# Kernel tuning notes

Measured on AMD Instinct MI355X. Metric: run time of the kernel, lower is better.

## Reference

```python
import jax, jax.numpy as jnp
import numpy as np

B, S, HID, NH = 2, 2048, 1024, 16
HD = HID // NH  # 64


def setup_inputs() -> dict:
    key = jax.random.key(0)
    ks = jax.random.split(key, 10)
    sc = 0.02
    return {
        "hidden_states": jax.random.normal(ks[0], (B, S, HID), jnp.float32),
        "attention_mask": jnp.zeros((B, 1, 1, S), jnp.float32),
        "struct_attn_mask": jax.random.normal(ks[1], (B, S, S), jnp.float32),
        "Wq": jax.random.normal(ks[2], (HID, HID), jnp.float32) * sc,
        "bq": jnp.zeros((HID,), jnp.float32),
        "Wk": jax.random.normal(ks[3], (HID, HID), jnp.float32) * sc,
        "bk": jnp.zeros((HID,), jnp.float32),
        "Wv": jax.random.normal(ks[4], (HID, HID), jnp.float32) * sc,
        "bv": jnp.zeros((HID,), jnp.float32),
        "struct_gate": jnp.full((NH,), 0.1, jnp.float32),
    }


def _heads(x):
    # [B,S,HID] -> [B,NH,S,HD]
    return x.reshape(B, S, NH, HD).transpose(0, 2, 1, 3)


def reference(hidden_states, attention_mask, struct_attn_mask, Wq, bq, Wk, bk, Wv, bv, struct_gate):
    q = _heads(hidden_states @ Wq.T + bq)
    k = _heads(hidden_states @ Wk.T + bk)
    v = _heads(hidden_states @ Wv.T + bv)
    scores = jnp.einsum("bhqd,bhkd->bhqk", q, k) / np.sqrt(HD).astype(np.float32)
    scores = scores + attention_mask
    scores = scores + struct_attn_mask[:, None, :, :] * struct_gate[None, :, None, None]
    probs = jax.nn.softmax(scores, axis=-1)  # dropout p=0 (eval) -> no-op
    ctx = jnp.einsum("bhqk,bhkd->bhqd", probs, v)
    ctx = ctx.transpose(0, 2, 1, 3).reshape(B, S, HID)
    return (ctx,)
```

## Files before the change

### kernel.cpp

```cpp
#include <hip/hip_runtime.h>
#include <hip/hip_bf16.h>
#include <cmath>

#define S_LEN 2048
#define HIDN  1024
#define NHEAD 16
#define HDIM  64
#define NBAT  2

static constexpr long NA = (long)NBAT * S_LEN * HIDN;
static constexpr long NW = (long)HIDN * HIDN;
static constexpr long NM = (long)NBAT * S_LEN * S_LEN;
static constexpr long NAM = (long)NBAT * S_LEN;

typedef __attribute__((ext_vector_type(8))) __bf16 bf16x8;
typedef __attribute__((ext_vector_type(4))) float f32x4;
typedef __attribute__((ext_vector_type(16))) float f32x16;
typedef __attribute__((ext_vector_type(4))) unsigned short u16x4;

#define LOG2E 1.44269504088896340736f

__device__ __forceinline__ unsigned short f2bf(float f) {
  __hip_bfloat16 h = __float2bfloat16(f);
  unsigned short u;
  __builtin_memcpy(&u, &h, 2);
  return u;
}

__device__ __forceinline__ float bfu2f(unsigned short u) {
  unsigned v = (unsigned)u << 16;
  float f;
  __builtin_memcpy(&f, &v, 4);
  return f;
}

__device__ __forceinline__ unsigned cvtpk(float a, float b) {
  unsigned r;
  asm volatile("v_cvt_pk_bf16_f32 %0, %1, %2" : "=v"(r) : "v"(a), "v"(b));
  return r;
}

__device__ __forceinline__ void gload_lds16(const void* g, void* l) {
  __builtin_amdgcn_global_load_lds(
      (const __attribute__((address_space(1))) void*)g,
      (__attribute__((address_space(3))) void*)l, 16, 0, 0);
}

__global__ __launch_bounds__(256) void convert_kernel(
    const float* __restrict__ hs, const float* __restrict__ wq,
    const float* __restrict__ wk, const float* __restrict__ wv,
    const float* __restrict__ mask, const float* __restrict__ amask,
    __hip_bfloat16* __restrict__ Abf, __hip_bfloat16* __restrict__ Wcat,
    __hip_bfloat16* __restrict__ Mbf, float* __restrict__ amg) {
  const long tot4 = (NA + 3 * NW + NM + NAM) >> 2;
  for (long i4 = (long)blockIdx.x * blockDim.x + threadIdx.x; i4 < tot4;
       i4 += (long)gridDim.x * blockDim.x) {
    long i = i4 << 2;
    if (i < NA + 3 * NW + NM) {
      const float* s;
      __hip_bfloat16* dq;
      if (i < NA)               { s = hs + i;                   dq = Abf + i; }
      else if (i < NA + NW)     { s = wq + (i - NA);            dq = Wcat + (i - NA); }
      else if (i < NA + 2 * NW) { s = wk + (i - NA - NW);       dq = Wcat + (i - NA); }
      else if (i < NA + 3 * NW) { s = wv + (i - NA - 2 * NW);   dq = Wcat + (i - NA); }
      else                      { s = mask + (i - NA - 3 * NW); dq = Mbf + (i - NA - 3 * NW); }
      float4 v = *(const float4*)s;
      union { unsigned short u[4]; uint2 p; } o;
      o.u[0] = f2bf(v.x); o.u[1] = f2bf(v.y); o.u[2] = f2bf(v.z); o.u[3] = f2bf(v.w);
      *(uint2*)dq = o.p;
    } else {
      long j = i - (NA + 3 * NW + NM);
      float4 v = *(const float4*)(amask + j);
      v.x *= LOG2E; v.y *= LOG2E; v.z *= LOG2E; v.w *= LOG2E;
      *(float4*)(amg + j) = v;
    }
  }
}

__global__ __launch_bounds__(256) void qkv_gemm(
    const __hip_bfloat16* __restrict__ A, const __hip_bfloat16* __restrict__ Bw,
    const float* __restrict__ bq, const float* __restrict__ bk,
    const float* __restrict__ bv, __hip_bfloat16* __restrict__ qb,
    __hip_bfloat16* __restrict__ kb, __hip_bfloat16* __restrict__ vb) {
  __shared__ __hip_bfloat16 sA[128 * 32];
  __shared__ __hip_bfloat16 sB[128 * 32];

  int bid = blockIdx.x;
  int cpx = gridDim.x >> 3;
  int wg = (bid & 7) * cpx + (bid >> 3);
  int bm = wg / 24, bn = wg % 24;
  int tid = threadIdx.x, lane = tid & 63, wid = tid >> 6;
  int wr = wid >> 1, wc = wid & 1;
  int lr = lane & 15, hi = lane >> 4;
  int srow = lane >> 2, scol = (lane & 3) * 8;

  f32x4 acc[4][4] = {};

  for (int kt = 0; kt < 32; ++kt) {
    int k0 = kt * 32;
#pragma unroll
    for (int cc = 0; cc < 2; ++cc) {
      int c = wid * 2 + cc;
      const __hip_bfloat16* ga =
          A + ((size_t)(bm * 128 + c * 16 + srow) * 1024 + k0 + scol);
      gload_lds16(ga, (char*)sA + c * 1024);
      const __hip_bfloat16* gb =
          Bw + ((size_t)(bn * 128 + c * 16 + srow) * 1024 + k0 + scol);
      gload_lds16(gb, (char*)sB + c * 1024);
    }
    __syncthreads();
    bf16x8 af[4], bf[4];
#pragma unroll
    for (int mt = 0; mt < 4; ++mt)
      af[mt] = *(const bf16x8*)((const char*)sA +
                                ((wr * 64 + mt * 16 + lr) * 32 + hi * 8) * 2);
#pragma unroll
    for (int nt = 0; nt < 4; ++nt)
      bf[nt] = *(const bf16x8*)((const char*)sB +
                                ((wc * 64 + nt * 16 + lr) * 32 + hi * 8) * 2);
#pragma unroll
    for (int mt = 0; mt < 4; ++mt)
#pragma unroll
      for (int nt = 0; nt < 4; ++nt)
        acc[mt][nt] =
            __builtin_amdgcn_mfma_f32_16x16x32_bf16(af[mt], bf[nt], acc[mt][nt], 0, 0, 0);
    __syncthreads();
  }

  const float c2 = LOG2E / 8.0f;
#pragma unroll
  for (int nt = 0; nt < 4; ++nt) {
    int nb = bn * 128 + wc * 64 + nt * 16;
    int t = nb >> 10;
    int rem = nb & 1023;
    const float* bp = (t == 0) ? bq : (t == 1) ? bk : bv;
    __hip_bfloat16* ob = (t == 0) ? qb : (t == 1) ? kb : vb;
    float scl = (t == 0) ? c2 : 1.0f;
    int h = rem >> 6, d0 = rem & 63;
    float bias = bp[rem + lr];
    int d = d0 + lr;
#pragma unroll
    for (int mt = 0; mt < 4; ++mt) {
#pragma unroll
      for (int r = 0; r < 4; ++r) {
        int m = bm * 128 + wr * 64 + mt * 16 + hi * 4 + r;
        int b = m >> 11, s = m & 2047;
        size_t off = (((size_t)(b * NHEAD + h)) * S_LEN + s) * HDIM + d;
        ob[off] = __float2bfloat16((acc[mt][nt][r] + bias) * scl);
      }
    }
  }
}

__global__ __launch_bounds__(256) void vtrans_kernel(
    const __hip_bfloat16* __restrict__ vb, __hip_bfloat16* __restrict__ vt) {
  __shared__ __hip_bfloat16 tile[64][72];
  int bh = blockIdx.x >> 5;
  int st = blockIdx.x & 31;
  int t = threadIdx.x;
  int r8 = t >> 3, c8 = (t & 7) * 8;
#pragma unroll
  for (int p = 0; p < 2; ++p) {
    int row = p * 32 + r8;
    bf16x8 v = *(const bf16x8*)(vb + ((size_t)bh * S_LEN + st * 64 + row) * HDIM + c8);
    *(bf16x8*)&tile[row][c8] = v;
  }
  __syncthreads();
#pragma unroll
  for (int p = 0; p < 2; ++p) {
    int d = p * 32 + r8;
    union { unsigned short u[8]; bf16x8 v; } o;
#pragma unroll
    for (int j = 0; j < 8; ++j) {
      __hip_bfloat16 e = tile[c8 + j][d];
      __builtin_memcpy(&o.u[j], &e, 2);
    }
    *(bf16x8*)(vt + ((size_t)bh * HDIM + d) * S_LEN + st * 64 + c8) = o.v;
  }
}

__global__ __launch_bounds__(512, 4) void attn_kernel(
    const __hip_bfloat16* __restrict__ qb, const __hip_bfloat16* __restrict__ kbuf,
    const __hip_bfloat16* __restrict__ vt, const __hip_bfloat16* __restrict__ Mbf,
    const float* __restrict__ amg, const float* __restrict__ gate,
    float* __restrict__ out) {
  __shared__ alignas(16) char smem[65536];
  __shared__ float mlb[4][2][32];

  int bid = blockIdx.x;
  int wg = (bid & 7) * 64 + (bid >> 3);
  int bi = wg >> 8;
  int h = (wg >> 4) & 15;
  int qt = wg & 15;
  int bh = bi * NHEAD + h;

  int tid = threadIdx.x;
  int lane = tid & 63, wid = tid >> 6;
  int grp = wid >> 2, w4 = wid & 3;
  int l31 = lane & 31, hi2 = lane >> 5;
  int qbase = qt * 128 + w4 * 32;
  int qrow = qbase + l31;
  int kbase = grp << 10;
  float g2 = gate[h] * LOG2E;

  const char* Kb = (const char*)kbuf + (size_t)bh * S_LEN * 128;
  const char* Vb = (const char*)vt + (size_t)bh * HDIM * S_LEN * 2;
  const char* Mq = (const char*)Mbf + ((size_t)bi * S_LEN + qbase) * S_LEN * 2;
  const float* abase = amg + (size_t)bi * S_LEN + hi2 * 4;

  bf16x8 qf[4];
  {
    const __hip_bfloat16* qp = qb + ((size_t)bh * S_LEN + qrow) * HDIM + hi2 * 8;
#pragma unroll
    for (int dc = 0; dc < 4; ++dc) qf[dc] = *(const bf16x8*)(qp + dc * 16);
  }

  int r8 = lane >> 3;
  int swzK = ((lane & 7) ^ r8) << 4;
  int r4 = lane >> 2;
  int swz64 = ((lane & 3) ^ (r4 & 3)) << 4;

  auto stage = [&](int buf, int t) {
    int k0 = kbase + t * 32;
    char* base = smem + buf * 8192 + grp * 4096 + w4 * 1024;
    gload_lds16(Kb + (size_t)(k0 + w4 * 8 + r8) * 128 + swzK, base);
    gload_lds16(Vb + (size_t)(w4 * 16 + r4) * 4096 + (size_t)k0 * 2 + swz64,
                base + 16384);
    char* mdst = smem + 32768 + buf * 16384 + wid * 2048;
#pragma unroll
    for (int c = 0; c < 2; ++c) {
      int mrow = c * 16 + r4;
      gload_lds16(Mq + (size_t)mrow * 4096 + (size_t)k0 * 2 + swz64,
                  mdst + c * 1024);
    }
  };

  f32x16 O = {};
  f32x16 O2 = {};
  float m = -INFINITY, l = 0.f;
  int rswzK = (l31 & 7) << 4;
  int rswz64 = (l31 & 3) << 4;

  stage(0, 0);
  __syncthreads();

  for (int kt = 0; kt < 32; ++kt) {
    int cur = kt & 1;
    if (kt < 31) stage(cur ^ 1, kt + 1);
    int k0 = kbase + kt * 32;

    const char* sKc = smem + cur * 8192 + grp * 4096;
    const char* sVc = sKc + 16384;
    const char* sMc = smem + 32768 + cur * 16384 + wid * 2048;

    f32x16 st = {};
#pragma unroll
    for (int dc = 0; dc < 4; ++dc) {
      bf16x8 kf = *(const bf16x8*)(sKc + l31 * 128 + ((dc * 32 + hi2 * 16) ^ rswzK));
      st = __builtin_amdgcn_mfma_f32_32x32x16_bf16(kf, qf[dc], st, 0, 0, 0);
    }

    float pmax = -3.4e38f;
#pragma unroll
    for (int rp = 0; rp < 4; ++rp) {
      float4 am = *(const float4*)(abase + k0 + rp * 8);
      union { u16x4 v; unsigned short e[4]; } mv;
      mv.v = *(const u16x4*)(sMc + l31 * 64 + ((rp * 16) ^ rswz64) + hi2 * 8);
      float s0 = fmaf(bfu2f(mv.e[0]), g2, st[rp * 4 + 0] + am.x);
      float s1 = fmaf(bfu2f(mv.e[1]), g2, st[rp * 4 + 1] + am.y);
      float s2 = fmaf(bfu2f(mv.e[2]), g2, st[rp * 4 + 2] + am.z);
      float s3 = fmaf(bfu2f(mv.e[3]), g2, st[rp * 4 + 3] + am.w);
      st[rp * 4 + 0] = s0; st[rp * 4 + 1] = s1;
      st[rp * 4 + 2] = s2; st[rp * 4 + 3] = s3;
      pmax = fmaxf(pmax, fmaxf(fmaxf(s0, s1), fmaxf(s2, s3)));
    }
    pmax = fmaxf(pmax, __shfl_xor(pmax, 32));

    if (__any(pmax > m + 8.f)) {
      float mnew = fmaxf(m, pmax);
      float alpha = exp2f(m - mnew);
      m = mnew;
      l *= alpha;
      O *= alpha;
      O2 *= alpha;
    }

    float rs0 = 0.f, rs1 = 0.f, rs2 = 0.f, rs3 = 0.f;
#pragma unroll
    for (int rp = 0; rp < 4; ++rp) {
      float p0 = exp2f(st[rp * 4 + 0] - m);
      float p1 = exp2f(st[rp * 4 + 1] - m);
      float p2 = exp2f(st[rp * 4 + 2] - m);
      float p3 = exp2f(st[rp * 4 + 3] - m);
      st[rp * 4 + 0] = p0; st[rp * 4 + 1] = p1;
      st[rp * 4 + 2] = p2; st[rp * 4 + 3] = p3;
      rs0 += p0; rs1 += p1; rs2 += p2; rs3 += p3;
    }
    float rs = (rs0 + rs1) + (rs2 + rs3);
    rs += __shfl_xor(rs, 32);
    l += rs;

#pragma unroll
    for (int ks = 0; ks < 2; ++ks) {
      int rp = ks * 2;
      unsigned A0 = cvtpk(st[rp * 4 + 0], st[rp * 4 + 1]);
      unsigned A1 = cvtpk(st[rp * 4 + 2], st[rp * 4 + 3]);
      unsigned B0 = cvtpk(st[rp * 4 + 4], st[rp * 4 + 5]);
      unsigned B1 = cvtpk(st[rp * 4 + 6], st[rp * 4 + 7]);
      asm volatile("v_permlane32_swap_b32 %0, %1" : "+v"(A0), "+v"(B0));
      asm volatile("v_permlane32_swap_b32 %0, %1" : "+v"(A1), "+v"(B1));
      union { unsigned w[4]; bf16x8 v; } Bf;
      Bf.w[0] = A0; Bf.w[1] = A1; Bf.w[2] = B0; Bf.w[3] = B1;
      bf16x8 v0 = *(const bf16x8*)(sVc + l31 * 64 + (((ks * 2 + hi2) << 4) ^ rswz64));
      bf16x8 v1 = *(const bf16x8*)(sVc + (32 + l31) * 64 + (((ks * 2 + hi2) << 4) ^ rswz64));
      O = __builtin_amdgcn_mfma_f32_32x32x16_bf16(v0, Bf.v, O, 0, 0, 0);
      O2 = __builtin_amdgcn_mfma_f32_32x32x16_bf16(v1, Bf.v, O2, 0, 0, 0);
    }
    __syncthreads();
  }

  float* mbuf = (float*)smem + w4 * (32 * 68);
  if (grp == 1) {
    if (hi2 == 0) { mlb[w4][0][l31] = m; mlb[w4][1][l31] = l; }
#pragma unroll
    for (int dt = 0; dt < 2; ++dt)
#pragma unroll
      for (int rq = 0; rq < 4; ++rq) {
        int d0 = dt * 32 + 8 * rq + 4 * hi2;
        const f32x16& Ox = dt ? O2 : O;
        f32x4 v = {Ox[rq * 4 + 0], Ox[rq * 4 + 1], Ox[rq * 4 + 2], Ox[rq * 4 + 3]};
        *(f32x4*)(mbuf + l31 * 68 + d0) = v;
      }
  }
  __syncthreads();
  if (grp == 0) {
    float m1 = mlb[w4][0][l31], l1 = mlb[w4][1][l31];
    float mx = fmaxf(m, m1);
    float a0 = exp2f(m - mx), a1 = exp2f(m1 - mx);
    float linv = 1.0f / (a0 * l + a1 * l1);
    a0 *= linv; a1 *= linv;
    float* orow = out + ((size_t)bi * S_LEN + qrow) * HIDN + h * HDIM;
#pragma unroll
    for (int dt = 0; dt < 2; ++dt)
#pragma unroll
      for (int rq = 0; rq < 4; ++rq) {
        int d0 = dt * 32 + 8 * rq + 4 * hi2;
        const f32x16& Ox = dt ? O2 : O;
        f32x4 v1 = *(const f32x4*)(mbuf + l31 * 68 + d0);
        float4 o;
        o.x = Ox[rq * 4 + 0] * a0 + v1[0] * a1;
        o.y = Ox[rq * 4 + 1] * a0 + v1[1] * a1;
        o.z = Ox[rq * 4 + 2] * a0 + v1[2] * a1;
        o.w = Ox[rq * 4 + 3] * a0 + v1[3] * a1;
        *(float4*)(orow + d0) = o;
      }
  }
}

extern "C" void kernel_launch(void* const* d_in, const int* in_sizes, int n_in,
                              void* d_out, int out_size, void* d_ws, size_t ws_size,
                              hipStream_t stream) {
  const float* hs    = (const float*)d_in[0];
  const float* amask = (const float*)d_in[1];
  const float* smask = (const float*)d_in[2];
  const float* Wq    = (const float*)d_in[3];
  const float* bq    = (const float*)d_in[4];
  const float* Wk    = (const float*)d_in[5];
  const float* bk    = (const float*)d_in[6];
  const float* Wv    = (const float*)d_in[7];
  const float* bv    = (const float*)d_in[8];
  const float* gate  = (const float*)d_in[9];

  char* ws = (char*)d_ws;
  __hip_bfloat16* Abf  = (__hip_bfloat16*)(ws);
  __hip_bfloat16* Wcat = (__hip_bfloat16*)(ws + 8388608);
  __hip_bfloat16* qb   = (__hip_bfloat16*)(ws + 8388608 + 6291456);
  __hip_bfloat16* kb   = qb + NA;
  __hip_bfloat16* vb   = kb + NA;
  __hip_bfloat16* Mbf  = vb + NA;
  float*          amg  = (float*)(Mbf + NM);
  __hip_bfloat16* vt   = Abf;

  convert_kernel<<<2048, 256, 0, stream>>>(hs, Wq, Wk, Wv, smask, amask, Abf, Wcat, Mbf, amg);
  qkv_gemm<<<768, 256, 0, stream>>>(Abf, Wcat, bq, bk, bv, qb, kb, vb);
  vtrans_kernel<<<1024, 256, 0, stream>>>(vb, vt);
  attn_kernel<<<512, 512, 0, stream>>>(qb, kb, vt, Mbf, amg, gate, (float*)d_out);
}
```

Before: 150.8 us.

## Stream struct mask via register prefetch, widen K/V tiles to 64, stage mask in LDS

The attention loop now processes 64 keys per barrier-separated stage, in two 32-key sub-steps, instead of 32 keys. This halves the number of __syncthreads and LDS staging rounds. The struct mask is no longer staged through LDS. Each lane loads its own row's mask values directly from global memory into registers, one stage ahead. The additive attention mask is loaded once into LDS instead of being read from global memory every iteration. Shared memory grows to about 72KB and register pressure rises from the prefetched mask, which may lower occupancy below the launch-bounds target.

```diff
diff --git a/kernel.cpp b/kernel.cpp
--- a/kernel.cpp
+++ b/kernel.cpp
@@ -184,7 +184,7 @@
     const __hip_bfloat16* __restrict__ vt, const __hip_bfloat16* __restrict__ Mbf,
     const float* __restrict__ amg, const float* __restrict__ gate,
     float* __restrict__ out) {
-  __shared__ alignas(16) char smem[65536];
+  __shared__ alignas(16) char smem[73728];
   __shared__ float mlb[4][2][32];
 
   int bid = blockIdx.x;
@@ -205,8 +205,7 @@
 
   const char* Kb = (const char*)kbuf + (size_t)bh * S_LEN * 128;
   const char* Vb = (const char*)vt + (size_t)bh * HDIM * S_LEN * 2;
-  const char* Mq = (const char*)Mbf + ((size_t)bi * S_LEN + qbase) * S_LEN * 2;
-  const float* abase = amg + (size_t)bi * S_LEN + hi2 * 4;
+  const char* Mrow = (const char*)Mbf + ((size_t)bi * S_LEN + qrow) * S_LEN * 2 + hi2 * 8;
 
   bf16x8 qf[4];
   {
@@ -215,106 +214,122 @@
     for (int dc = 0; dc < 4; ++dc) qf[dc] = *(const bf16x8*)(qp + dc * 16);
   }
 
-  int r8 = lane >> 3;
-  int swzK = ((lane & 7) ^ r8) << 4;
-  int r4 = lane >> 2;
-  int swz64 = ((lane & 3) ^ (r4 & 3)) << 4;
+  int r8 = lane >> 3, ch = lane & 7;
+  float* amL = (float*)(smem + 65536 + grp * 4096);
 
   auto stage = [&](int buf, int t) {
-    int k0 = kbase + t * 32;
-    char* base = smem + buf * 8192 + grp * 4096 + w4 * 1024;
-    gload_lds16(Kb + (size_t)(k0 + w4 * 8 + r8) * 128 + swzK, base);
-    gload_lds16(Vb + (size_t)(w4 * 16 + r4) * 4096 + (size_t)k0 * 2 + swz64,
-                base + 16384);
-    char* mdst = smem + 32768 + buf * 16384 + wid * 2048;
+    int k0 = kbase + t * 64;
+    char* kdst = smem + buf * 32768 + grp * 16384 + w4 * 2048;
+    char* vdst = kdst + 8192;
 #pragma unroll
     for (int c = 0; c < 2; ++c) {
-      int mrow = c * 16 + r4;
-      gload_lds16(Mq + (size_t)mrow * 4096 + (size_t)k0 * 2 + swz64,
-                  mdst + c * 1024);
+      int row = w4 * 16 + c * 8 + r8;
+      gload_lds16(Kb + (size_t)(k0 + row) * 128 + ((ch ^ r8) << 4), kdst + c * 1024);
+      gload_lds16(Vb + (size_t)row * 4096 + (size_t)k0 * 2 + ((ch ^ r8) << 4),
+                  vdst + c * 1024);
     }
   };
 
-  f32x16 O = {};
-  f32x16 O2 = {};
+  u16x4 mn0[4], mn1[4];
+#pragma unroll
+  for (int rp = 0; rp < 4; ++rp) {
+    mn0[rp] = *(const u16x4*)(Mrow + (size_t)(kbase + rp * 8) * 2);
+    mn1[rp] = *(const u16x4*)(Mrow + (size_t)(kbase + 32 + rp * 8) * 2);
+  }
+
+  stage(0, 0);
+  gload_lds16((const char*)amg + ((size_t)bi * S_LEN + kbase + w4 * 256) * 4,
+              (char*)amL + w4 * 1024);
+  __syncthreads();
+
+  f32x16 O = {}, O2 = {};
   float m = -INFINITY, l = 0.f;
-  int rswzK = (l31 & 7) << 4;
-  int rswz64 = (l31 & 3) << 4;
-
-  stage(0, 0);
-  __syncthreads();
-
-  for (int kt = 0; kt < 32; ++kt) {
-    int cur = kt & 1;
-    if (kt < 31) stage(cur ^ 1, kt + 1);
-    int k0 = kbase + kt * 32;
-
-    const char* sKc = smem + cur * 8192 + grp * 4096;
-    const char* sVc = sKc + 16384;
-    const char* sMc = smem + 32768 + cur * 16384 + wid * 2048;
-
-    f32x16 st = {};
-#pragma unroll
-    for (int dc = 0; dc < 4; ++dc) {
-      bf16x8 kf = *(const bf16x8*)(sKc + l31 * 128 + ((dc * 32 + hi2 * 16) ^ rswzK));
-      st = __builtin_amdgcn_mfma_f32_32x32x16_bf16(kf, qf[dc], st, 0, 0, 0);
-    }
-
-    float pmax = -3.4e38f;
-#pragma unroll
-    for (int rp = 0; rp < 4; ++rp) {
-      float4 am = *(const float4*)(abase + k0 + rp * 8);
-      union { u16x4 v; unsigned short e[4]; } mv;
-      mv.v = *(const u16x4*)(sMc + l31 * 64 + ((rp * 16) ^ rswz64) + hi2 * 8);
-      float s0 = fmaf(bfu2f(mv.e[0]), g2, st[rp * 4 + 0] + am.x);
-      float s1 = fmaf(bfu2f(mv.e[1]), g2, st[rp * 4 + 1] + am.y);
-      float s2 = fmaf(bfu2f(mv.e[2]), g2, st[rp * 4 + 2] + am.z);
-      float s3 = fmaf(bfu2f(mv.e[3]), g2, st[rp * 4 + 3] + am.w);
-      st[rp * 4 + 0] = s0; st[rp * 4 + 1] = s1;
-      st[rp * 4 + 2] = s2; st[rp * 4 + 3] = s3;
-      pmax = fmaxf(pmax, fmaxf(fmaxf(s0, s1), fmaxf(s2, s3)));
-    }
-    pmax = fmaxf(pmax, __shfl_xor(pmax, 32));
-
-    if (__any(pmax > m + 8.f)) {
-      float mnew = fmaxf(m, pmax);
-      float alpha = exp2f(m - mnew);
-      m = mnew;
-      l *= alpha;
-      O *= alpha;
-      O2 *= alpha;
-    }
-
-    float rs0 = 0.f, rs1 = 0.f, rs2 = 0.f, rs3 = 0.f;
-#pragma unroll
-    for (int rp = 0; rp < 4; ++rp) {
-      float p0 = exp2f(st[rp * 4 + 0] - m);
-      float p1 = exp2f(st[rp * 4 + 1] - m);
-      float p2 = exp2f(st[rp * 4 + 2] - m);
-      float p3 = exp2f(st[rp * 4 + 3] - m);
-      st[rp * 4 + 0] = p0; st[rp * 4 + 1] = p1;
-      st[rp * 4 + 2] = p2; st[rp * 4 + 3] = p3;
-      rs0 += p0; rs1 += p1; rs2 += p2; rs3 += p3;
-    }
-    float rs = (rs0 + rs1) + (rs2 + rs3);
-    rs += __shfl_xor(rs, 32);
-    l += rs;
-
-#pragma unroll
-    for (int ks = 0; ks < 2; ++ks) {
-      int rp = ks * 2;
-      unsigned A0 = cvtpk(st[rp * 4 + 0], st[rp * 4 + 1]);
-      unsigned A1 = cvtpk(st[rp * 4 + 2], st[rp * 4 + 3]);
-      unsigned B0 = cvtpk(st[rp * 4 + 4], st[rp * 4 + 5]);
-      unsigned B1 = cvtpk(st[rp * 4 + 6], st[rp * 4 + 7]);
-      asm volatile("v_permlane32_swap_b32 %0, %1" : "+v"(A0), "+v"(B0));
-      asm volatile("v_permlane32_swap_b32 %0, %1" : "+v"(A1), "+v"(B1));
-      union { unsigned w[4]; bf16x8 v; } Bf;
-      Bf.w[0] = A0; Bf.w[1] = A1; Bf.w[2] = B0; Bf.w[3] = B1;
-      bf16x8 v0 = *(const bf16x8*)(sVc + l31 * 64 + (((ks * 2 + hi2) << 4) ^ rswz64));
-      bf16x8 v1 = *(const bf16x8*)(sVc + (32 + l31) * 64 + (((ks * 2 + hi2) << 4) ^ rswz64));
-      O = __builtin_amdgcn_mfma_f32_32x32x16_bf16(v0, Bf.v, O, 0, 0, 0);
-      O2 = __builtin_amdgcn_mfma_f32_32x32x16_bf16(v1, Bf.v, O2, 0, 0, 0);
+
+  for (int t = 0; t < 16; ++t) {
+    int cur = t & 1;
+    if (t < 15) stage(cur ^ 1, t + 1);
+    const char* sK = smem + cur * 32768 + grp * 16384;
+    const char* sV = sK + 8192;
+
+#pragma unroll
+    for (int ss = 0; ss < 2; ++ss) {
+      int klocal = t * 64 + ss * 32;
+
+      f32x16 st = {};
+#pragma unroll
+      for (int dc = 0; dc < 4; ++dc) {
+        int row = ss * 32 + l31;
+        bf16x8 kf = *(const bf16x8*)(sK + row * 128 +
+                                     (((dc * 2 + hi2) ^ (l31 & 7)) << 4));
+        st = __builtin_amdgcn_mfma_f32_32x32x16_bf16(kf, qf[dc], st, 0, 0, 0);
+      }
+
+      float pmax = -3.4e38f;
+#pragma unroll
+      for (int rp = 0; rp < 4; ++rp) {
+        float4 am = *(const float4*)(amL + klocal + rp * 8 + hi2 * 4);
+        union { u16x4 v; unsigned short e[4]; } mv;
+        mv.v = ss ? mn1[rp] : mn0[rp];
+        float s0 = fmaf(bfu2f(mv.e[0]), g2, st[rp * 4 + 0] + am.x);
+        float s1 = fmaf(bfu2f(mv.e[1]), g2, st[rp * 4 + 1] + am.y);
+        float s2 = fmaf(bfu2f(mv.e[2]), g2, st[rp * 4 + 2] + am.z);
+        float s3 = fmaf(bfu2f(mv.e[3]), g2, st[rp * 4 + 3] + am.w);
+        st[rp * 4 + 0] = s0; st[rp * 4 + 1] = s1;
+        st[rp * 4 + 2] = s2; st[rp * 4 + 3] = s3;
+        pmax = fmaxf(pmax, fmaxf(fmaxf(s0, s1), fmaxf(s2, s3)));
+      }
+
+      if (t < 15) {
+        int kn = kbase + (t + 1) * 64 + ss * 32;
+#pragma unroll
+        for (int rp = 0; rp < 4; ++rp) {
+          u16x4 nv = *(const u16x4*)(Mrow + (size_t)(kn + rp * 8) * 2);
+          if (ss) mn1[rp] = nv; else mn0[rp] = nv;
+        }
+      }
+
+      pmax = fmaxf(pmax, __shfl_xor(pmax, 32));
+      if (__any(pmax > m + 8.f)) {
+        float mnew = fmaxf(m, pmax);
+        float alpha = exp2f(m - mnew);
+        m = mnew;
+        l *= alpha;
+        O *= alpha;
+        O2 *= alpha;
+      }
+
+      float rs0 = 0.f, rs1 = 0.f, rs2 = 0.f, rs3 = 0.f;
+#pragma unroll
+      for (int rp = 0; rp < 4; ++rp) {
+        float p0 = exp2f(st[rp * 4 + 0] - m);
+        float p1 = exp2f(st[rp * 4 + 1] - m);
+        float p2 = exp2f(st[rp * 4 + 2] - m);
+        float p3 = exp2f(st[rp * 4 + 3] - m);
+        st[rp * 4 + 0] = p0; st[rp * 4 + 1] = p1;
+        st[rp * 4 + 2] = p2; st[rp * 4 + 3] = p3;
+        rs0 += p0; rs1 += p1; rs2 += p2; rs3 += p3;
+      }
+      float rs = (rs0 + rs1) + (rs2 + rs3);
+      rs += __shfl_xor(rs, 32);
+      l += rs;
+
+#pragma unroll
+      for (int ks = 0; ks < 2; ++ks) {
+        int rp = ks * 2;
+        unsigned A0 = cvtpk(st[rp * 4 + 0], st[rp * 4 + 1]);
+        unsigned A1 = cvtpk(st[rp * 4 + 2], st[rp * 4 + 3]);
+        unsigned B0 = cvtpk(st[rp * 4 + 4], st[rp * 4 + 5]);
+        unsigned B1 = cvtpk(st[rp * 4 + 6], st[rp * 4 + 7]);
+        asm volatile("v_permlane32_swap_b32 %0, %1" : "+v"(A0), "+v"(B0));
+        asm volatile("v_permlane32_swap_b32 %0, %1" : "+v"(A1), "+v"(B1));
+        union { unsigned w[4]; bf16x8 v; } Bf;
+        Bf.w[0] = A0; Bf.w[1] = A1; Bf.w[2] = B0; Bf.w[3] = B1;
+        int vc = ss * 4 + ks * 2 + hi2;
+        bf16x8 v0 = *(const bf16x8*)(sV + l31 * 128 + ((vc ^ (l31 & 7)) << 4));
+        bf16x8 v1 = *(const bf16x8*)(sV + (32 + l31) * 128 + ((vc ^ (l31 & 7)) << 4));
+        O = __builtin_amdgcn_mfma_f32_32x32x16_bf16(v0, Bf.v, O, 0, 0, 0);
+        O2 = __builtin_amdgcn_mfma_f32_32x32x16_bf16(v1, Bf.v, O2, 0, 0, 0);
+      }
     }
     __syncthreads();
   }
```

After: 144.6 us. 1.04x faster.
